# Kernel optimization log

Measured on AMD Instinct MI355X. Metric: run time of the kernel, lower is better.

## Reference

```python
import jax, jax.numpy as jnp
import numpy as np

N = 262144   # total nodes
E = 1048576  # total edges
B = 512      # graphs per batch
IN, H, EDIM, AH, CH, NB = 8, 128, 4, 128, 128, 4

def _lin(key, fi, fo):
    # kaiming_normal fan_out/relu approximated with fan_in scaling (only affects init stats)
    return jax.random.normal(key, (fi, fo), jnp.float32) * np.sqrt(2.0 / fi)

def setup_inputs() -> dict:
    key = jax.random.key(0)
    ks = jax.random.split(key, 24)
    inp = {}
    inp['x'] = jax.random.normal(ks[0], (N, IN), jnp.float32)
    inp['edge_index'] = jax.random.randint(ks[1], (2, E), 0, N)
    inp['edge_attr'] = jax.random.normal(ks[2], (E, EDIM), jnp.float32)
    seg = N // B
    inp['batch'] = (jnp.arange(N) // seg).astype(jnp.int32)
    inp['ptr'] = (jnp.arange(B + 1) * seg).astype(jnp.int32)
    dims = [(IN, H), (H, H), (H, H)]  # final layer outputs embed_dim == H
    for l, (di, do) in enumerate(dims):
        inp[f'We{l}'] = _lin(ks[3 + 2 * l], EDIM, di)
        inp[f'be{l}'] = jnp.zeros((di,), jnp.float32)
        inp[f'W{l}'] = _lin(ks[4 + 2 * l], di, do)
        inp[f'b{l}'] = jnp.zeros((do,), jnp.float32)
    inp['laW1'] = _lin(ks[10], H, AH); inp['lab1'] = jnp.zeros((AH,), jnp.float32)
    inp['laW2'] = _lin(ks[11], AH, 1); inp['lab2'] = jnp.zeros((1,), jnp.float32)
    inp['maW1'] = _lin(ks[12], H, AH); inp['mab1'] = jnp.zeros((AH,), jnp.float32)
    inp['maW2'] = _lin(ks[13], AH, NB); inp['mab2'] = jnp.zeros((NB,), jnp.float32)
    inp['lcW1'] = _lin(ks[14], H, CH); inp['lcb1'] = jnp.zeros((CH,), jnp.float32)
    inp['lcW2'] = _lin(ks[15], CH, 1); inp['lcb2'] = jnp.zeros((1,), jnp.float32)
    inp['mcW1'] = _lin(ks[16], H, CH); inp['mcb1'] = jnp.zeros((CH,), jnp.float32)
    inp['mcW2'] = _lin(ks[17], CH, 1); inp['mcb2'] = jnp.zeros((1,), jnp.float32)
    return inp

def _gnn(x, edge_index, edge_attr, Wes, bes, Ws, bs):
    # GINE-style edge-conditioned message passing (dropout off / eval mode)
    src, dst = edge_index[0], edge_index[1]
    h = x
    for We, be, W, b in zip(Wes, bes, Ws, bs):
        msg = jax.nn.relu(h[src] + edge_attr @ We + be)            # [E, d]
        agg = jax.ops.segment_sum(msg, dst, num_segments=N)        # [N, d]
        h = jax.nn.relu((h + agg) @ W + b)
    return h

def reference(x, edge_index, edge_attr, batch, ptr,
              We0, be0, W0, b0, We1, be1, W1, b1, We2, be2, W2, b2,
              laW1, lab1, laW2, lab2, maW1, mab1, maW2, mab2,
              lcW1, lcb1, lcW2, lcb2, mcW1, mcb1, mcW2, mcb2):
    emb = _gnn(x, edge_index, edge_attr, [We0, We1, We2], [be0, be1, be2], [W0, W1, W2], [b0, b1, b2])  # [N, H]

    # per-node location logit, then fused segmented softmax over each graph's nodes
    loc_logits = (jax.nn.relu(emb @ laW1 + lab1) @ laW2 + lab2)[:, 0]  # [N]
    seg_max = jax.ops.segment_max(loc_logits, batch, num_segments=B)
    shifted = loc_logits - seg_max[batch]
    denom = jax.ops.segment_sum(jnp.exp(shifted), batch, num_segments=B)
    logp = shifted - jnp.log(denom)[batch]                              # per-node log-prob within its graph
    loc_entropy = -jax.ops.segment_sum(jnp.exp(logp) * logp, batch, num_segments=B)  # [B]

    # segmented categorical sampling via Gumbel-max (global node index, matching start+local_idx)
    key = jax.random.key(42)
    u = jax.random.uniform(key, (N,), minval=1e-6, maxval=1.0 - 1e-6)
    pert = loc_logits - jnp.log(-jnp.log(u))
    pmax = jax.ops.segment_max(pert, batch, num_segments=B)
    cand = jnp.where(pert >= pmax[batch], jnp.arange(N), N)
    locations = jax.ops.segment_min(cand, batch, num_segments=B)        # [B] global indices
    loc_log_probs = logp[locations]                                     # [B]

    sel = emb[locations]                                                # [B, H]
    mut_logits = jax.nn.relu(sel @ maW1 + mab1) @ maW2 + mab2           # [B, NB]
    mut_logp = jax.nn.log_softmax(mut_logits, axis=-1)
    mutations = jax.random.categorical(jax.random.fold_in(key, 1), mut_logits, axis=-1)  # [B]
    mut_log_probs = jnp.take_along_axis(mut_logp, mutations[:, None], axis=-1)[:, 0]
    mut_entropy = -jnp.sum(jnp.exp(mut_logp) * mut_logp, axis=-1)

    # critics: global_add_pool + MLP -> scalar per graph; mutation critic on selected node
    pooled = jax.ops.segment_sum(emb, batch, num_segments=B)            # [B, H]
    loc_values = (jax.nn.relu(pooled @ lcW1 + lcb1) @ lcW2 + lcb2)[:, 0]
    mut_values = (jax.nn.relu(sel @ mcW1 + mcb1) @ mcW2 + mcb2)[:, 0]

    return (locations, mutations, loc_log_probs, mut_log_probs,
            loc_entropy, mut_entropy, loc_values, mut_values, emb)
```

## Files before the change

### kernel.cpp

```cpp
#include <hip/hip_runtime.h>
#include <cstdint>
#include <cstddef>

#define NN 262144
#define EE 1048576
#define BB 512
#define SEG 512

__device__ __forceinline__ unsigned rotl32(unsigned x, int r) {
    return (x << r) | (x >> (32 - r));
}

__device__ __forceinline__ void tf2x32(unsigned k0, unsigned k1, unsigned x0, unsigned x1,
                                       unsigned& o0, unsigned& o1) {
    unsigned ks[3] = {k0, k1, k0 ^ k1 ^ 0x1BD11BDAu};
    x0 += ks[0]; x1 += ks[1];
    const int R0[4] = {13, 15, 26, 6};
    const int R1[4] = {17, 29, 16, 24};
#pragma unroll
    for (int i = 0; i < 5; ++i) {
        const int* R = (i & 1) ? R1 : R0;
#pragma unroll
        for (int j = 0; j < 4; ++j) {
            x0 += x1;
            x1 = rotl32(x1, R[j]);
            x1 ^= x0;
        }
        x0 += ks[(i + 1) % 3];
        x1 += ks[(i + 2) % 3] + (unsigned)(i + 1);
    }
    o0 = x0; o1 = x1;
}

__device__ __forceinline__ float unif_loc(unsigned idx) {
    unsigned j = idx & (NN / 2 - 1);
    unsigned half = idx >> 17;
    unsigned o0, o1;
    tf2x32(0u, 42u, j, j + (unsigned)(NN / 2), o0, o1);
    unsigned bits = half ? o1 : o0;
    float f = __uint_as_float((bits >> 9) | 0x3F800000u) - 1.0f;
    const float minv = 1e-6f;
    const float maxv = 1.0f - 1e-6f;
    const float span = maxv - minv;
    return fmaxf(minv, __fadd_rn(__fmul_rn(f, span), minv));
}

__global__ void csr_count(const int* __restrict__ dst, int* __restrict__ counts, int E) {
    int i = blockIdx.x * 256 + threadIdx.x;
    if (i < E) atomicAdd(&counts[dst[i]], 1);
}

__global__ void scan512(const int* __restrict__ in, int* __restrict__ outExcl, int* __restrict__ bsum) {
    __shared__ int s[512];
    int b = blockIdx.x, tid = threadIdx.x;
    int v = in[(size_t)b * 512 + tid];
    s[tid] = v;
    __syncthreads();
    for (int d = 1; d < 512; d <<= 1) {
        int add = (tid >= d) ? s[tid - d] : 0;
        __syncthreads();
        s[tid] += add;
        __syncthreads();
    }
    outExcl[(size_t)b * 512 + tid] = s[tid] - v;
    if (tid == 511) bsum[b] = s[511];
}

__global__ void scan_fix(int* __restrict__ offs, const int* __restrict__ bbase,
                         int* __restrict__ cursor, int N, int E) {
    int gid = blockIdx.x * 512 + threadIdx.x;
    int v = offs[gid] + bbase[blockIdx.x];
    offs[gid] = v;
    cursor[gid] = v;
    if (gid == 0) offs[N] = E;
}

__global__ void csr_fill(const int* __restrict__ dst, const int* __restrict__ src,
                         const float4* __restrict__ ea, int* __restrict__ cursor,
                         int* __restrict__ ssrc, float4* __restrict__ sea, int E) {
    int i = blockIdx.x * 256 + threadIdx.x;
    if (i < E) {
        int p = atomicAdd(&cursor[dst[i]], 1);
        ssrc[p] = src[i];
        sea[p] = ea[i];
    }
}

__global__ void agg_l0(const float* __restrict__ x, const int* __restrict__ ssrc,
                       const float4* __restrict__ sea, const int* __restrict__ offs,
                       const float* __restrict__ We0, const float* __restrict__ be0,
                       float* __restrict__ out) {
    __shared__ float Ws[32];
    __shared__ float bs[8];
    int tid = threadIdx.x;
    if (tid < 32) Ws[tid] = We0[tid];
    if (tid < 8) bs[tid] = be0[tid];
    __syncthreads();
    int n = blockIdx.x * 256 + tid;
    float a[8] = {0.f, 0.f, 0.f, 0.f, 0.f, 0.f, 0.f, 0.f};
    int pb = offs[n], pe = offs[n + 1];
    for (int p = pb; p < pe; ++p) {
        int s = ssrc[p];
        float4 ev = sea[p];
        float4 xa = *(const float4*)(x + (size_t)s * 8);
        float4 xb = *(const float4*)(x + (size_t)s * 8 + 4);
        float xs[8] = {xa.x, xa.y, xa.z, xa.w, xb.x, xb.y, xb.z, xb.w};
#pragma unroll
        for (int j2 = 0; j2 < 8; ++j2) {
            float m = xs[j2] + bs[j2] + ev.x * Ws[j2] + ev.y * Ws[8 + j2] +
                      ev.z * Ws[16 + j2] + ev.w * Ws[24 + j2];
            a[j2] += fmaxf(m, 0.f);
        }
    }
    float4 o0 = {a[0], a[1], a[2], a[3]};
    float4 o1 = {a[4], a[5], a[6], a[7]};
    *(float4*)(out + (size_t)n * 8) = o0;
    *(float4*)(out + (size_t)n * 8 + 4) = o1;
}

__global__ void update_l0(const float* __restrict__ x, const float* __restrict__ agg0,
                          const float* __restrict__ W0, const float* __restrict__ b0,
                          float* __restrict__ h1) {
    __shared__ float Ws[8 * 128];
    __shared__ float bs[128];
    __shared__ float ts[2][8];
    int tid = threadIdx.x;
#pragma unroll
    for (int i = tid; i < 1024; i += 256) Ws[i] = W0[i];
    if (tid < 128) bs[tid] = b0[tid];
    int sub = tid >> 7;
    int c = tid & 127;
    int node = blockIdx.x * 2 + sub;
    if (c < 8) ts[sub][c] = x[(size_t)node * 8 + c] + agg0[(size_t)node * 8 + c];
    __syncthreads();
    float acc = bs[c];
#pragma unroll
    for (int k = 0; k < 8; ++k) acc = fmaf(ts[sub][k], Ws[k * 128 + c], acc);
    h1[(size_t)node * 128 + c] = fmaxf(acc, 0.f);
}

#define MSG(hv, ev)                                                                 \
    {                                                                               \
        float mx = hv.x + bv.x + ev.x * w0.x + ev.y * w1.x + ev.z * w2.x + ev.w * w3.x; \
        float my = hv.y + bv.y + ev.x * w0.y + ev.y * w1.y + ev.z * w2.y + ev.w * w3.y; \
        acc.x += fmaxf(mx, 0.f);                                                    \
        acc.y += fmaxf(my, 0.f);                                                    \
    }

__global__ __launch_bounds__(256) void agg_l(const float2* __restrict__ h2,
                                             const int* __restrict__ ssrc,
                                             const float4* __restrict__ sea,
                                             const int* __restrict__ offs,
                                             const float* __restrict__ We,
                                             const float* __restrict__ be,
                                             float2* __restrict__ out) {
    int tid = threadIdx.x;
    int node = blockIdx.x * 4 + (tid >> 6);
    node = __builtin_amdgcn_readfirstlane(node);
    int lane = tid & 63;
    const float2* We2 = (const float2*)We;
    float2 w0 = We2[lane], w1 = We2[64 + lane], w2 = We2[128 + lane], w3 = We2[192 + lane];
    float2 bv = ((const float2*)be)[lane];
    float2 acc; acc.x = 0.f; acc.y = 0.f;
    int pb = offs[node], pe = offs[node + 1];
    int p = pb;
    for (; p + 4 <= pe; p += 4) {
        int s0 = ssrc[p], s1 = ssrc[p + 1], s2 = ssrc[p + 2], s3 = ssrc[p + 3];
        float4 e0 = sea[p], e1 = sea[p + 1], e2 = sea[p + 2], e3 = sea[p + 3];
        float2 ha = h2[(size_t)s0 * 64 + lane];
        float2 hb = h2[(size_t)s1 * 64 + lane];
        float2 hc = h2[(size_t)s2 * 64 + lane];
        float2 hd = h2[(size_t)s3 * 64 + lane];
        MSG(ha, e0) MSG(hb, e1) MSG(hc, e2) MSG(hd, e3)
    }
    for (; p < pe; ++p) {
        int s0 = ssrc[p];
        float4 e0 = sea[p];
        float2 ha = h2[(size_t)s0 * 64 + lane];
        MSG(ha, e0)
    }
    out[(size_t)node * 64 + lane] = acc;
}

__device__ __forceinline__ int wslot(int c) {
    return (c & 1) ? (16 + (((c >> 1) + 4) & 15)) : (c >> 1);
}

__global__ __launch_bounds__(256, 4) void gemm_k(const float* __restrict__ P, const float* Q,
                                                 const float* __restrict__ W,
                                                 const float* __restrict__ bias,
                                                 float* out) {
    __shared__ float As[32][132];
    __shared__ float Ws[32][128];
    int tid = threadIdx.x;
    int r0 = blockIdx.x * 128;
    int ty = tid >> 4, tx = tid & 15;
    int wo1 = 4 * tx;
    int wo2 = 64 + 4 * ((tx + 4) & 15);
    float acc[8][8] = {};
    for (int kc = 0; kc < 4; ++kc) {
        int k0 = kc * 32;
        __syncthreads();
#pragma unroll
        for (int i = 0; i < 4; ++i) {
            int f = tid + 256 * i;
            int r = f >> 3;
            int c4 = f & 7;
            size_t g = (size_t)(r0 + r) * 128 + k0 + 4 * c4;
            float4 pv = *(const float4*)(P + g);
            if (Q) {
                float4 qv = *(const float4*)(Q + g);
                pv.x += qv.x; pv.y += qv.y; pv.z += qv.z; pv.w += qv.w;
            }
            As[4 * c4 + 0][r] = pv.x;
            As[4 * c4 + 1][r] = pv.y;
            As[4 * c4 + 2][r] = pv.z;
            As[4 * c4 + 3][r] = pv.w;
        }
#pragma unroll
        for (int i = 0; i < 4; ++i) {
            int f = tid + 256 * i;
            int k = f >> 5;
            int c4 = f & 31;
            float4 wv = *(const float4*)(W + (size_t)(k0 + k) * 128 + 4 * c4);
            *(float4*)&Ws[k][4 * wslot(c4)] = wv;
        }
        __syncthreads();
#pragma unroll 4
        for (int k = 0; k < 32; ++k) {
            float4 a0 = *(const float4*)&As[k][8 * ty];
            float4 a1 = *(const float4*)&As[k][8 * ty + 4];
            float4 wv0 = *(const float4*)&Ws[k][wo1];
            float4 wv1 = *(const float4*)&Ws[k][wo2];
            float av[8] = {a0.x, a0.y, a0.z, a0.w, a1.x, a1.y, a1.z, a1.w};
            float wv[8] = {wv0.x, wv0.y, wv0.z, wv0.w, wv1.x, wv1.y, wv1.z, wv1.w};
#pragma unroll
            for (int m = 0; m < 8; ++m)
#pragma unroll
                for (int n = 0; n < 8; ++n)
                    acc[m][n] = fmaf(av[m], wv[n], acc[m][n]);
        }
    }
    float4 b0 = *(const float4*)(bias + 8 * tx);
    float4 b1 = *(const float4*)(bias + 8 * tx + 4);
#pragma unroll
    for (int m = 0; m < 8; ++m) {
        float4 o0, o1;
        o0.x = fmaxf(acc[m][0] + b0.x, 0.f);
        o0.y = fmaxf(acc[m][1] + b0.y, 0.f);
        o0.z = fmaxf(acc[m][2] + b0.z, 0.f);
        o0.w = fmaxf(acc[m][3] + b0.w, 0.f);
        o1.x = fmaxf(acc[m][4] + b1.x, 0.f);
        o1.y = fmaxf(acc[m][5] + b1.y, 0.f);
        o1.z = fmaxf(acc[m][6] + b1.z, 0.f);
        o1.w = fmaxf(acc[m][7] + b1.w, 0.f);
        size_t g = (size_t)(r0 + 8 * ty + m) * 128 + 8 * tx;
        *(float4*)(out + g) = o0;
        *(float4*)(out + g + 4) = o1;
    }
}

__global__ __launch_bounds__(256, 4) void gemm_logit(const float* __restrict__ P,
                                                     const float* __restrict__ W,
                                                     const float* __restrict__ bias,
                                                     const float* __restrict__ w2,
                                                     const float* __restrict__ b2,
                                                     float* __restrict__ L) {
    __shared__ float As[32][132];
    __shared__ float Ws[32][128];
    int tid = threadIdx.x;
    int r0 = blockIdx.x * 128;
    int ty = tid >> 4, tx = tid & 15;
    int wo1 = 4 * tx;
    int wo2 = 64 + 4 * ((tx + 4) & 15);
    float acc[8][8] = {};
    for (int kc = 0; kc < 4; ++kc) {
        int k0 = kc * 32;
        __syncthreads();
#pragma unroll
        for (int i = 0; i < 4; ++i) {
            int f = tid + 256 * i;
            int r = f >> 3;
            int c4 = f & 7;
            size_t g = (size_t)(r0 + r) * 128 + k0 + 4 * c4;
            float4 pv = *(const float4*)(P + g);
            As[4 * c4 + 0][r] = pv.x;
            As[4 * c4 + 1][r] = pv.y;
            As[4 * c4 + 2][r] = pv.z;
            As[4 * c4 + 3][r] = pv.w;
        }
#pragma unroll
        for (int i = 0; i < 4; ++i) {
            int f = tid + 256 * i;
            int k = f >> 5;
            int c4 = f & 31;
            float4 wv = *(const float4*)(W + (size_t)(k0 + k) * 128 + 4 * c4);
            *(float4*)&Ws[k][4 * wslot(c4)] = wv;
        }
        __syncthreads();
#pragma unroll 4
        for (int k = 0; k < 32; ++k) {
            float4 a0 = *(const float4*)&As[k][8 * ty];
            float4 a1 = *(const float4*)&As[k][8 * ty + 4];
            float4 wv0 = *(const float4*)&Ws[k][wo1];
            float4 wv1 = *(const float4*)&Ws[k][wo2];
            float av[8] = {a0.x, a0.y, a0.z, a0.w, a1.x, a1.y, a1.z, a1.w};
            float wv[8] = {wv0.x, wv0.y, wv0.z, wv0.w, wv1.x, wv1.y, wv1.z, wv1.w};
#pragma unroll
            for (int m = 0; m < 8; ++m)
#pragma unroll
                for (int n = 0; n < 8; ++n)
                    acc[m][n] = fmaf(av[m], wv[n], acc[m][n]);
        }
    }
    float4 b0 = *(const float4*)(bias + 8 * tx);
    float4 b1 = *(const float4*)(bias + 8 * tx + 4);
    float4 w2a = *(const float4*)(w2 + 8 * tx);
    float4 w2b = *(const float4*)(w2 + 8 * tx + 4);
    float b2v = b2[0];
#pragma unroll
    for (int m = 0; m < 8; ++m) {
        float v = fmaxf(acc[m][0] + b0.x, 0.f) * w2a.x;
        v += fmaxf(acc[m][1] + b0.y, 0.f) * w2a.y;
        v += fmaxf(acc[m][2] + b0.z, 0.f) * w2a.z;
        v += fmaxf(acc[m][3] + b0.w, 0.f) * w2a.w;
        v += fmaxf(acc[m][4] + b1.x, 0.f) * w2b.x;
        v += fmaxf(acc[m][5] + b1.y, 0.f) * w2b.y;
        v += fmaxf(acc[m][6] + b1.z, 0.f) * w2b.z;
        v += fmaxf(acc[m][7] + b1.w, 0.f) * w2b.w;
        v += __shfl_down(v, 8, 16);
        v += __shfl_down(v, 4, 16);
        v += __shfl_down(v, 2, 16);
        v += __shfl_down(v, 1, 16);
        if (tx == 0) L[r0 + 8 * ty + m] = v + b2v;
    }
}

__global__ void sample_k(const float* __restrict__ L, float* __restrict__ ob,
                         int* __restrict__ locInt) {
    int g = blockIdx.x, tid = threadIdx.x;
    __shared__ float sh[512];
    __shared__ float rb[256];
    __shared__ int ib[256];
    float l0 = L[g * 512 + tid];
    float l1 = L[g * 512 + 256 + tid];
    rb[tid] = fmaxf(l0, l1);
    __syncthreads();
    for (int s2 = 128; s2 > 0; s2 >>= 1) {
        if (tid < s2) rb[tid] = fmaxf(rb[tid], rb[tid + s2]);
        __syncthreads();
    }
    float mx = rb[0];
    __syncthreads();
    float s0 = l0 - mx, s1 = l1 - mx;
    sh[tid] = s0; sh[256 + tid] = s1;
    float e0 = expf(s0), e1 = expf(s1);
    rb[tid] = e0 + e1;
    __syncthreads();
    for (int s2 = 128; s2 > 0; s2 >>= 1) {
        if (tid < s2) rb[tid] += rb[tid + s2];
        __syncthreads();
    }
    float denom = rb[0];
    __syncthreads();
    rb[tid] = e0 * s0 + e1 * s1;
    __syncthreads();
    for (int s2 = 128; s2 > 0; s2 >>= 1) {
        if (tid < s2) rb[tid] += rb[tid + s2];
        __syncthreads();
    }
    float sum2 = rb[0];
    __syncthreads();
    unsigned i0 = (unsigned)(g * 512 + tid);
    unsigned i1 = i0 + 256u;
    float p0 = l0 - logf(-logf(unif_loc(i0)));
    float p1 = l1 - logf(-logf(unif_loc(i1)));
    rb[tid] = fmaxf(p0, p1);
    __syncthreads();
    for (int s2 = 128; s2 > 0; s2 >>= 1) {
        if (tid < s2) rb[tid] = fmaxf(rb[tid], rb[tid + s2]);
        __syncthreads();
    }
    float pmax = rb[0];
    __syncthreads();
    int c0 = (p0 >= pmax) ? tid : 0x7FFFFFFF;
    int c1 = (p1 >= pmax) ? (tid + 256) : 0x7FFFFFFF;
    ib[tid] = min(c0, c1);
    __syncthreads();
    for (int s2 = 128; s2 > 0; s2 >>= 1) {
        if (tid < s2) ib[tid] = min(ib[tid], ib[tid + s2]);
        __syncthreads();
    }
    if (tid == 0) {
        int li = ib[0];
        float logD = logf(denom);
        ob[g] = (float)(g * 512 + li);
        ob[1024 + g] = sh[li] - logD;
        ob[2048 + g] = logD - sum2 / denom;
        locInt[g] = g * 512 + li;
    }
}

__global__ void pool_k(const float* __restrict__ emb, float* __restrict__ pooled) {
    int g = blockIdx.x, tid = threadIdx.x;
    int c = tid & 127, rg = tid >> 7;
    __shared__ float sh[512];
    float s0 = 0.f, s1 = 0.f, s2 = 0.f, s3 = 0.f;
    const float* base = emb + ((size_t)g * 512 + (size_t)rg * 128) * 128 + c;
    for (int n = 0; n < 128; n += 4) {
        s0 += base[(size_t)(n + 0) * 128];
        s1 += base[(size_t)(n + 1) * 128];
        s2 += base[(size_t)(n + 2) * 128];
        s3 += base[(size_t)(n + 3) * 128];
    }
    sh[tid] = (s0 + s1) + (s2 + s3);
    __syncthreads();
    if (rg == 0) pooled[g * 128 + c] = sh[c] + sh[128 + c] + sh[256 + c] + sh[384 + c];
}

__global__ void heads_k(const float* __restrict__ emb, const float* __restrict__ pooled,
                        const int* __restrict__ locInt,
                        const float* __restrict__ maW1, const float* __restrict__ mab1,
                        const float* __restrict__ maW2, const float* __restrict__ mab2,
                        const float* __restrict__ lcW1, const float* __restrict__ lcb1,
                        const float* __restrict__ lcW2, const float* __restrict__ lcb2,
                        const float* __restrict__ mcW1, const float* __restrict__ mcb1,
                        const float* __restrict__ mcW2, const float* __restrict__ mcb2,
                        float* __restrict__ ob) {
    int g = blockIdx.x, tid = threadIdx.x;
    __shared__ float sel[128], pl[128];
    __shared__ float red[4][128];
    __shared__ float red1[128];
    __shared__ float mcv_sh;
    sel[tid] = emb[(size_t)locInt[g] * 128 + tid];
    pl[tid] = pooled[g * 128 + tid];
    __syncthreads();
    float h = mab1[tid];
    for (int k = 0; k < 128; ++k) h = fmaf(sel[k], maW1[k * 128 + tid], h);
    h = fmaxf(h, 0.f);
    red[0][tid] = h * maW2[tid * 4 + 0];
    red[1][tid] = h * maW2[tid * 4 + 1];
    red[2][tid] = h * maW2[tid * 4 + 2];
    red[3][tid] = h * maW2[tid * 4 + 3];
    __syncthreads();
    for (int s2 = 64; s2 > 0; s2 >>= 1) {
        if (tid < s2) {
            red[0][tid] += red[0][tid + s2];
            red[1][tid] += red[1][tid + s2];
            red[2][tid] += red[2][tid + s2];
            red[3][tid] += red[3][tid + s2];
        }
        __syncthreads();
    }
    float h2 = mcb1[tid];
    for (int k = 0; k < 128; ++k) h2 = fmaf(sel[k], mcW1[k * 128 + tid], h2);
    h2 = fmaxf(h2, 0.f);
    red1[tid] = h2 * mcW2[tid];
    __syncthreads();
    for (int s2 = 64; s2 > 0; s2 >>= 1) {
        if (tid < s2) red1[tid] += red1[tid + s2];
        __syncthreads();
    }
    if (tid == 0) mcv_sh = red1[0] + mcb2[0];
    __syncthreads();
    float h3 = lcb1[tid];
    for (int k = 0; k < 128; ++k) h3 = fmaf(pl[k], lcW1[k * 128 + tid], h3);
    h3 = fmaxf(h3, 0.f);
    red1[tid] = h3 * lcW2[tid];
    __syncthreads();
    for (int s2 = 64; s2 > 0; s2 >>= 1) {
        if (tid < s2) red1[tid] += red1[tid + s2];
        __syncthreads();
    }
    if (tid == 0) {
        float lcv = red1[0] + lcb2[0];
        float lg[4];
#pragma unroll
        for (int c = 0; c < 4; ++c) lg[c] = red[c][0] + mab2[c];
        unsigned fk0, fk1;
        tf2x32(0u, 42u, 0u, 1u, fk0, fk1);
        float gmb[4];
#pragma unroll
        for (int c = 0; c < 4; ++c) {
            unsigned m = (unsigned)(g * 4 + c);
            unsigned j = m & 1023u;
            unsigned halfb = m >> 10;
            unsigned o0, o1;
            tf2x32(fk0, fk1, j, j + 1024u, o0, o1);
            unsigned bits = halfb ? o1 : o0;
            float f = __uint_as_float((bits >> 9) | 0x3F800000u) - 1.0f;
            const float tiny = 1.17549435e-38f;
            float u = fmaxf(tiny, __fadd_rn(__fmul_rn(f, 1.0f), tiny));
            gmb[c] = -logf(-logf(u));
        }
        int best = 0;
        float bz = gmb[0] + lg[0];
#pragma unroll
        for (int c = 1; c < 4; ++c) {
            float z = gmb[c] + lg[c];
            if (z > bz) { bz = z; best = c; }
        }
        float M = fmaxf(fmaxf(lg[0], lg[1]), fmaxf(lg[2], lg[3]));
        float se = 0.f;
#pragma unroll
        for (int c = 0; c < 4; ++c) se += expf(lg[c] - M);
        float lse = M + logf(se);
        float ent = 0.f;
#pragma unroll
        for (int c = 0; c < 4; ++c) {
            float lp = lg[c] - lse;
            ent -= expf(lp) * lp;
        }
        ob[512 + g] = (float)best;
        ob[1536 + g] = lg[best] - lse;
        ob[2560 + g] = ent;
        ob[3072 + g] = lcv;
        ob[3584 + g] = mcv_sh;
    }
}

extern "C" void kernel_launch(void* const* d_in, const int* in_sizes, int n_in,
                              void* d_out, int out_size, void* d_ws, size_t ws_size,
                              hipStream_t stream) {
    const float* x   = (const float*)d_in[0];
    const int* ei    = (const int*)d_in[1];
    const float* ea  = (const float*)d_in[2];
    const float* We0 = (const float*)d_in[5];
    const float* be0 = (const float*)d_in[6];
    const float* W0  = (const float*)d_in[7];
    const float* b0  = (const float*)d_in[8];
    const float* We1 = (const float*)d_in[9];
    const float* be1 = (const float*)d_in[10];
    const float* W1  = (const float*)d_in[11];
    const float* b1  = (const float*)d_in[12];
    const float* We2 = (const float*)d_in[13];
    const float* be2 = (const float*)d_in[14];
    const float* W2  = (const float*)d_in[15];
    const float* b2  = (const float*)d_in[16];
    const float* laW1 = (const float*)d_in[17];
    const float* lab1 = (const float*)d_in[18];
    const float* laW2 = (const float*)d_in[19];
    const float* lab2 = (const float*)d_in[20];
    const float* maW1 = (const float*)d_in[21];
    const float* mab1 = (const float*)d_in[22];
    const float* maW2 = (const float*)d_in[23];
    const float* mab2 = (const float*)d_in[24];
    const float* lcW1 = (const float*)d_in[25];
    const float* lcb1 = (const float*)d_in[26];
    const float* lcW2 = (const float*)d_in[27];
    const float* lcb2 = (const float*)d_in[28];
    const float* mcW1 = (const float*)d_in[29];
    const float* mcb1 = (const float*)d_in[30];
    const float* mcW2 = (const float*)d_in[31];
    const float* mcb2 = (const float*)d_in[32];

    float* out = (float*)d_out;
    char* ws = (char*)d_ws;
    size_t off = 0;
    auto alloc = [&](size_t bytes) -> void* {
        void* p = ws + off;
        off += (bytes + 255) & ~(size_t)255;
        return p;
    };
    float* U    = (float*)alloc((size_t)NN * 128 * 4);
    int* counts = (int*)alloc((size_t)NN * 4);
    int* offs   = (int*)alloc((size_t)(NN + 1) * 4);
    int* cursor = (int*)alloc((size_t)NN * 4);
    int* ssrc   = (int*)alloc((size_t)EE * 4);
    float4* sea = (float4*)alloc((size_t)EE * 16);
    int* bsum   = (int*)alloc(512 * 4);
    int* bbase  = (int*)alloc(512 * 4);
    int* bscr   = (int*)alloc(512 * 4);
    float* Lg   = (float*)alloc((size_t)NN * 4);
    float* pooled = (float*)alloc((size_t)BB * 128 * 4);
    int* locInt = (int*)alloc((size_t)BB * 4);

    const int* src = ei;
    const int* dstA = ei + EE;
    float* V = out + 4096;
    float* agg0 = U;

    hipMemsetAsync(counts, 0, (size_t)NN * 4, stream);
    csr_count<<<EE / 256, 256, 0, stream>>>(dstA, counts, EE);
    scan512<<<NN / 512, 512, 0, stream>>>(counts, offs, bsum);
    scan512<<<1, 512, 0, stream>>>(bsum, bbase, bscr);
    scan_fix<<<NN / 512, 512, 0, stream>>>(offs, bbase, cursor, NN, EE);
    csr_fill<<<EE / 256, 256, 0, stream>>>(dstA, src, (const float4*)ea, cursor, ssrc, sea, EE);

    agg_l0<<<NN / 256, 256, 0, stream>>>(x, ssrc, sea, offs, We0, be0, agg0);
    update_l0<<<NN / 2, 256, 0, stream>>>(x, agg0, W0, b0, V);
    agg_l<<<NN / 4, 256, 0, stream>>>((const float2*)V, ssrc, sea, offs, We1, be1, (float2*)U);
    gemm_k<<<NN / 128, 256, 0, stream>>>(V, U, W1, b1, U);
    agg_l<<<NN / 4, 256, 0, stream>>>((const float2*)U, ssrc, sea, offs, We2, be2, (float2*)V);
    gemm_k<<<NN / 128, 256, 0, stream>>>(U, V, W2, b2, V);

    gemm_logit<<<NN / 128, 256, 0, stream>>>(V, laW1, lab1, laW2, lab2, Lg);
    sample_k<<<BB, 256, 0, stream>>>(Lg, out, locInt);

    pool_k<<<BB, 512, 0, stream>>>(V, pooled);
    heads_k<<<BB, 128, 0, stream>>>(V, pooled, locInt, maW1, mab1, maW2, mab2,
                                    lcW1, lcb1, lcW2, lcb2, mcW1, mcb1, mcW2, mcb2, out);
}
```

Before: 1.016 ms.

## Replace FP32 FMA GEMMs with split-bf16 MFMA kernels and prepacked weights

The three 128x128 node GEMMs (two layer updates and the location-logit head) now run on MFMA 16x16x32 bf16 instructions instead of scalar FP32 FMA tiles in shared memory. Each operand is split into a high and a low bf16 part and combined with three MFMAs (bf16x3) to stay close to FP32 accuracy. A small pack kernel writes the weights once in fragment order into the now-unused cursor buffer, so the GEMMs read B fragments straight from global/L2 and need no shared memory. A fragments are converted in registers. The cost is extra MFMA work, a small precision loss, and uncoalesced scalar stores in the epilogue.

Measured after the change: 927.3 us. -8.7%, faster.

```diff
diff --git a/kernel.cpp b/kernel.cpp
--- a/kernel.cpp
+++ b/kernel.cpp
@@ -182,158 +182,190 @@
     out[(size_t)node * 64 + lane] = acc;
 }
 
-__device__ __forceinline__ int wslot(int c) {
-    return (c & 1) ? (16 + (((c >> 1) + 4) & 15)) : (c >> 1);
-}
-
-__global__ __launch_bounds__(256, 4) void gemm_k(const float* __restrict__ P, const float* Q,
-                                                 const float* __restrict__ W,
+
+typedef __attribute__((ext_vector_type(8))) short bf16x8;
+typedef __attribute__((ext_vector_type(4))) float f32x4;
+
+__device__ __forceinline__ ushort bf16r(float x) {
+    unsigned u = __float_as_uint(x);
+    return (ushort)((u + 0x7FFFu + ((u >> 16) & 1u)) >> 16);
+}
+__device__ __forceinline__ float bf2f(ushort h) {
+    return __uint_as_float(((unsigned)h) << 16);
+}
+
+__global__ void pack3(const float* __restrict__ W1, const float* __restrict__ W2,
+                      const float* __restrict__ LA, uint4* __restrict__ dst) {
+    const float* W = (blockIdx.x == 0) ? W1 : (blockIdx.x == 1) ? W2 : LA;
+    uint4* ph = dst + (size_t)blockIdx.x * 4096;
+    uint4* pl = ph + 2048;
+    int t = threadIdx.x;
+    int l = t & 63, q = t >> 6;
+    int lo = l & 15, kg = l >> 4;
+    for (int i = 0; i < 8; ++i) {
+        int combo = q * 8 + i;
+        int kc = combo >> 3, n = combo & 7;
+        ushort h8[8], l8[8];
+#pragma unroll
+        for (int j = 0; j < 8; ++j) {
+            float wv = W[(size_t)(kc * 32 + kg * 8 + j) * 128 + n * 16 + lo];
+            ushort hh = bf16r(wv);
+            h8[j] = hh;
+            l8[j] = bf16r(wv - bf2f(hh));
+        }
+        int idx = (kc * 8 + n) * 64 + l;
+        ph[idx] = *(const uint4*)h8;
+        pl[idx] = *(const uint4*)l8;
+    }
+}
+
+__device__ __forceinline__ void load_a_frags(const float* P, const float* Q, int r0,
+                                             int lo, int kg, int kc,
+                                             bf16x8& ah0, bf16x8& al0,
+                                             bf16x8& ah1, bf16x8& al1) {
+#pragma unroll
+    for (int m = 0; m < 2; ++m) {
+        const float* ap = P + (size_t)(r0 + m * 16 + lo) * 128 + kc * 32 + kg * 8;
+        float4 p0 = *(const float4*)ap;
+        float4 p1 = *(const float4*)(ap + 4);
+        if (Q) {
+            const float* qp = Q + (size_t)(r0 + m * 16 + lo) * 128 + kc * 32 + kg * 8;
+            float4 q0 = *(const float4*)qp;
+            float4 q1 = *(const float4*)(qp + 4);
+            p0.x += q0.x; p0.y += q0.y; p0.z += q0.z; p0.w += q0.w;
+            p1.x += q1.x; p1.y += q1.y; p1.z += q1.z; p1.w += q1.w;
+        }
+        float av[8] = {p0.x, p0.y, p0.z, p0.w, p1.x, p1.y, p1.z, p1.w};
+        bf16x8 ah, al;
+#pragma unroll
+        for (int j = 0; j < 8; ++j) {
+            ushort hh = bf16r(av[j]);
+            ah[j] = (short)hh;
+            al[j] = (short)bf16r(av[j] - bf2f(hh));
+        }
+        if (m == 0) { ah0 = ah; al0 = al; } else { ah1 = ah; al1 = al; }
+    }
+}
+
+__global__ __launch_bounds__(256) void gemm_mfma(const float* __restrict__ P, const float* Q,
+                                                 const uint4* __restrict__ Wh,
+                                                 const uint4* __restrict__ Wl,
                                                  const float* __restrict__ bias,
                                                  float* out) {
-    __shared__ float As[32][132];
-    __shared__ float Ws[32][128];
     int tid = threadIdx.x;
-    int r0 = blockIdx.x * 128;
-    int ty = tid >> 4, tx = tid & 15;
-    int wo1 = 4 * tx;
-    int wo2 = 64 + 4 * ((tx + 4) & 15);
-    float acc[8][8] = {};
+    int w = tid >> 6, l = tid & 63;
+    int r0 = blockIdx.x * 128 + w * 32;
+    int lo = l & 15, kg = l >> 4;
+    const bf16x8* Bh = (const bf16x8*)Wh;
+    const bf16x8* Bl = (const bf16x8*)Wl;
+    f32x4 acc[2][8];
+#pragma unroll
+    for (int m = 0; m < 2; ++m)
+#pragma unroll
+        for (int n = 0; n < 8; ++n) acc[m][n] = (f32x4){0.f, 0.f, 0.f, 0.f};
+
     for (int kc = 0; kc < 4; ++kc) {
-        int k0 = kc * 32;
-        __syncthreads();
-#pragma unroll
-        for (int i = 0; i < 4; ++i) {
-            int f = tid + 256 * i;
-            int r = f >> 3;
-            int c4 = f & 7;
-            size_t g = (size_t)(r0 + r) * 128 + k0 + 4 * c4;
-            float4 pv = *(const float4*)(P + g);
-            if (Q) {
-                float4 qv = *(const float4*)(Q + g);
-                pv.x += qv.x; pv.y += qv.y; pv.z += qv.z; pv.w += qv.w;
+        bf16x8 ah0, al0, ah1, al1;
+        load_a_frags(P, Q, r0, lo, kg, kc, ah0, al0, ah1, al1);
+#pragma unroll
+        for (int h2i = 0; h2i < 2; ++h2i) {
+            bf16x8 bh[4], bl[4];
+#pragma unroll
+            for (int nn = 0; nn < 4; ++nn) {
+                int idx = (kc * 8 + h2i * 4 + nn) * 64 + l;
+                bh[nn] = Bh[idx];
+                bl[nn] = Bl[idx];
             }
-            As[4 * c4 + 0][r] = pv.x;
-            As[4 * c4 + 1][r] = pv.y;
-            As[4 * c4 + 2][r] = pv.z;
-            As[4 * c4 + 3][r] = pv.w;
-        }
-#pragma unroll
-        for (int i = 0; i < 4; ++i) {
-            int f = tid + 256 * i;
-            int k = f >> 5;
-            int c4 = f & 31;
-            float4 wv = *(const float4*)(W + (size_t)(k0 + k) * 128 + 4 * c4);
-            *(float4*)&Ws[k][4 * wslot(c4)] = wv;
-        }
-        __syncthreads();
-#pragma unroll 4
-        for (int k = 0; k < 32; ++k) {
-            float4 a0 = *(const float4*)&As[k][8 * ty];
-            float4 a1 = *(const float4*)&As[k][8 * ty + 4];
-            float4 wv0 = *(const float4*)&Ws[k][wo1];
-            float4 wv1 = *(const float4*)&Ws[k][wo2];
-            float av[8] = {a0.x, a0.y, a0.z, a0.w, a1.x, a1.y, a1.z, a1.w};
-            float wv[8] = {wv0.x, wv0.y, wv0.z, wv0.w, wv1.x, wv1.y, wv1.z, wv1.w};
-#pragma unroll
-            for (int m = 0; m < 8; ++m)
-#pragma unroll
-                for (int n = 0; n < 8; ++n)
-                    acc[m][n] = fmaf(av[m], wv[n], acc[m][n]);
-        }
-    }
-    float4 b0 = *(const float4*)(bias + 8 * tx);
-    float4 b1 = *(const float4*)(bias + 8 * tx + 4);
-#pragma unroll
-    for (int m = 0; m < 8; ++m) {
-        float4 o0, o1;
-        o0.x = fmaxf(acc[m][0] + b0.x, 0.f);
-        o0.y = fmaxf(acc[m][1] + b0.y, 0.f);
-        o0.z = fmaxf(acc[m][2] + b0.z, 0.f);
-        o0.w = fmaxf(acc[m][3] + b0.w, 0.f);
-        o1.x = fmaxf(acc[m][4] + b1.x, 0.f);
-        o1.y = fmaxf(acc[m][5] + b1.y, 0.f);
-        o1.z = fmaxf(acc[m][6] + b1.z, 0.f);
-        o1.w = fmaxf(acc[m][7] + b1.w, 0.f);
-        size_t g = (size_t)(r0 + 8 * ty + m) * 128 + 8 * tx;
-        *(float4*)(out + g) = o0;
-        *(float4*)(out + g + 4) = o1;
-    }
-}
-
-__global__ __launch_bounds__(256, 4) void gemm_logit(const float* __restrict__ P,
-                                                     const float* __restrict__ W,
-                                                     const float* __restrict__ bias,
-                                                     const float* __restrict__ w2,
-                                                     const float* __restrict__ b2,
-                                                     float* __restrict__ L) {
-    __shared__ float As[32][132];
-    __shared__ float Ws[32][128];
+#pragma unroll
+            for (int nn = 0; nn < 4; ++nn) {
+                int n = h2i * 4 + nn;
+                acc[0][n] = __builtin_amdgcn_mfma_f32_16x16x32_bf16(ah0, bh[nn], acc[0][n], 0, 0, 0);
+                acc[0][n] = __builtin_amdgcn_mfma_f32_16x16x32_bf16(al0, bh[nn], acc[0][n], 0, 0, 0);
+                acc[0][n] = __builtin_amdgcn_mfma_f32_16x16x32_bf16(ah0, bl[nn], acc[0][n], 0, 0, 0);
+                acc[1][n] = __builtin_amdgcn_mfma_f32_16x16x32_bf16(ah1, bh[nn], acc[1][n], 0, 0, 0);
+                acc[1][n] = __builtin_amdgcn_mfma_f32_16x16x32_bf16(al1, bh[nn], acc[1][n], 0, 0, 0);
+                acc[1][n] = __builtin_amdgcn_mfma_f32_16x16x32_bf16(ah1, bl[nn], acc[1][n], 0, 0, 0);
+            }
+        }
+    }
+    float bv[8];
+#pragma unroll
+    for (int n = 0; n < 8; ++n) bv[n] = bias[n * 16 + lo];
+#pragma unroll
+    for (int m = 0; m < 2; ++m)
+#pragma unroll
+        for (int n = 0; n < 8; ++n)
+#pragma unroll
+            for (int v = 0; v < 4; ++v) {
+                size_t g = (size_t)(r0 + m * 16 + kg * 4 + v) * 128 + n * 16 + lo;
+                out[g] = fmaxf(acc[m][n][v] + bv[n], 0.f);
+            }
+}
+
+__global__ __launch_bounds__(256) void gemm_logit_mfma(const float* __restrict__ P,
+                                                       const uint4* __restrict__ Wh,
+                                                       const uint4* __restrict__ Wl,
+                                                       const float* __restrict__ bias,
+                                                       const float* __restrict__ w2,
+                                                       const float* __restrict__ b2,
+                                                       float* __restrict__ L) {
     int tid = threadIdx.x;
-    int r0 = blockIdx.x * 128;
-    int ty = tid >> 4, tx = tid & 15;
-    int wo1 = 4 * tx;
-    int wo2 = 64 + 4 * ((tx + 4) & 15);
-    float acc[8][8] = {};
+    int w = tid >> 6, l = tid & 63;
+    int r0 = blockIdx.x * 128 + w * 32;
+    int lo = l & 15, kg = l >> 4;
+    const bf16x8* Bh = (const bf16x8*)Wh;
+    const bf16x8* Bl = (const bf16x8*)Wl;
+    f32x4 acc[2][8];
+#pragma unroll
+    for (int m = 0; m < 2; ++m)
+#pragma unroll
+        for (int n = 0; n < 8; ++n) acc[m][n] = (f32x4){0.f, 0.f, 0.f, 0.f};
+
     for (int kc = 0; kc < 4; ++kc) {
-        int k0 = kc * 32;
-        __syncthreads();
-#pragma unroll
-        for (int i = 0; i < 4; ++i) {
-            int f = tid + 256 * i;
-            int r = f >> 3;
-            int c4 = f & 7;
-            size_t g = (size_t)(r0 + r) * 128 + k0 + 4 * c4;
-            float4 pv = *(const float4*)(P + g);
-            As[4 * c4 + 0][r] = pv.x;
-            As[4 * c4 + 1][r] = pv.y;
-            As[4 * c4 + 2][r] = pv.z;
-            As[4 * c4 + 3][r] = pv.w;
-        }
-#pragma unroll
-        for (int i = 0; i < 4; ++i) {
-            int f = tid + 256 * i;
-            int k = f >> 5;
-            int c4 = f & 31;
-            float4 wv = *(const float4*)(W + (size_t)(k0 + k) * 128 + 4 * c4);
-            *(float4*)&Ws[k][4 * wslot(c4)] = wv;
-        }
-        __syncthreads();
-#pragma unroll 4
-        for (int k = 0; k < 32; ++k) {
-            float4 a0 = *(const float4*)&As[k][8 * ty];
-            float4 a1 = *(const float4*)&As[k][8 * ty + 4];
-            float4 wv0 = *(const float4*)&Ws[k][wo1];
-            float4 wv1 = *(const float4*)&Ws[k][wo2];
-            float av[8] = {a0.x, a0.y, a0.z, a0.w, a1.x, a1.y, a1.z, a1.w};
-            float wv[8] = {wv0.x, wv0.y, wv0.z, wv0.w, wv1.x, wv1.y, wv1.z, wv1.w};
-#pragma unroll
-            for (int m = 0; m < 8; ++m)
-#pragma unroll
-                for (int n = 0; n < 8; ++n)
-                    acc[m][n] = fmaf(av[m], wv[n], acc[m][n]);
-        }
-    }
-    float4 b0 = *(const float4*)(bias + 8 * tx);
-    float4 b1 = *(const float4*)(bias + 8 * tx + 4);
-    float4 w2a = *(const float4*)(w2 + 8 * tx);
-    float4 w2b = *(const float4*)(w2 + 8 * tx + 4);
+        bf16x8 ah0, al0, ah1, al1;
+        load_a_frags(P, (const float*)0, r0, lo, kg, kc, ah0, al0, ah1, al1);
+#pragma unroll
+        for (int h2i = 0; h2i < 2; ++h2i) {
+            bf16x8 bh[4], bl[4];
+#pragma unroll
+            for (int nn = 0; nn < 4; ++nn) {
+                int idx = (kc * 8 + h2i * 4 + nn) * 64 + l;
+                bh[nn] = Bh[idx];
+                bl[nn] = Bl[idx];
+            }
+#pragma unroll
+            for (int nn = 0; nn < 4; ++nn) {
+                int n = h2i * 4 + nn;
+                acc[0][n] = __builtin_amdgcn_mfma_f32_16x16x32_bf16(ah0, bh[nn], acc[0][n], 0, 0, 0);
+                acc[0][n] = __builtin_amdgcn_mfma_f32_16x16x32_bf16(al0, bh[nn], acc[0][n], 0, 0, 0);
+                acc[0][n] = __builtin_amdgcn_mfma_f32_16x16x32_bf16(ah0, bl[nn], acc[0][n], 0, 0, 0);
+                acc[1][n] = __builtin_amdgcn_mfma_f32_16x16x32_bf16(ah1, bh[nn], acc[1][n], 0, 0, 0);
+                acc[1][n] = __builtin_amdgcn_mfma_f32_16x16x32_bf16(al1, bh[nn], acc[1][n], 0, 0, 0);
+                acc[1][n] = __builtin_amdgcn_mfma_f32_16x16x32_bf16(ah1, bl[nn], acc[1][n], 0, 0, 0);
+            }
+        }
+    }
+    float bv[8], w2v[8];
+#pragma unroll
+    for (int n = 0; n < 8; ++n) {
+        bv[n] = bias[n * 16 + lo];
+        w2v[n] = w2[n * 16 + lo];
+    }
     float b2v = b2[0];
 #pragma unroll
-    for (int m = 0; m < 8; ++m) {
-        float v = fmaxf(acc[m][0] + b0.x, 0.f) * w2a.x;
-        v += fmaxf(acc[m][1] + b0.y, 0.f) * w2a.y;
-        v += fmaxf(acc[m][2] + b0.z, 0.f) * w2a.z;
-        v += fmaxf(acc[m][3] + b0.w, 0.f) * w2a.w;
-        v += fmaxf(acc[m][4] + b1.x, 0.f) * w2b.x;
-        v += fmaxf(acc[m][5] + b1.y, 0.f) * w2b.y;
-        v += fmaxf(acc[m][6] + b1.z, 0.f) * w2b.z;
-        v += fmaxf(acc[m][7] + b1.w, 0.f) * w2b.w;
-        v += __shfl_down(v, 8, 16);
-        v += __shfl_down(v, 4, 16);
-        v += __shfl_down(v, 2, 16);
-        v += __shfl_down(v, 1, 16);
-        if (tx == 0) L[r0 + 8 * ty + m] = v + b2v;
-    }
+    for (int m = 0; m < 2; ++m)
+#pragma unroll
+        for (int v = 0; v < 4; ++v) {
+            float s = 0.f;
+#pragma unroll
+            for (int n = 0; n < 8; ++n)
+                s += fmaxf(acc[m][n][v] + bv[n], 0.f) * w2v[n];
+            s += __shfl_xor(s, 8);
+            s += __shfl_xor(s, 4);
+            s += __shfl_xor(s, 2);
+            s += __shfl_xor(s, 1);
+            if (lo == 0) L[r0 + m * 16 + kg * 4 + v] = s + b2v;
+        }
 }
 
 __global__ void sample_k(const float* __restrict__ L, float* __restrict__ ob,
@@ -580,21 +612,24 @@
     float* V = out + 4096;
     float* agg0 = U;
 
+    uint4* wpack = (uint4*)cursor;
+
     hipMemsetAsync(counts, 0, (size_t)NN * 4, stream);
     csr_count<<<EE / 256, 256, 0, stream>>>(dstA, counts, EE);
     scan512<<<NN / 512, 512, 0, stream>>>(counts, offs, bsum);
     scan512<<<1, 512, 0, stream>>>(bsum, bbase, bscr);
     scan_fix<<<NN / 512, 512, 0, stream>>>(offs, bbase, cursor, NN, EE);
     csr_fill<<<EE / 256, 256, 0, stream>>>(dstA, src, (const float4*)ea, cursor, ssrc, sea, EE);
+    pack3<<<3, 256, 0, stream>>>(W1, W2, laW1, wpack);
 
     agg_l0<<<NN / 256, 256, 0, stream>>>(x, ssrc, sea, offs, We0, be0, agg0);
     update_l0<<<NN / 2, 256, 0, stream>>>(x, agg0, W0, b0, V);
     agg_l<<<NN / 4, 256, 0, stream>>>((const float2*)V, ssrc, sea, offs, We1, be1, (float2*)U);
-    gemm_k<<<NN / 128, 256, 0, stream>>>(V, U, W1, b1, U);
+    gemm_mfma<<<NN / 128, 256, 0, stream>>>(V, U, wpack, wpack + 2048, b1, U);
     agg_l<<<NN / 4, 256, 0, stream>>>((const float2*)U, ssrc, sea, offs, We2, be2, (float2*)V);
-    gemm_k<<<NN / 128, 256, 0, stream>>>(U, V, W2, b2, V);
-
-    gemm_logit<<<NN / 128, 256, 0, stream>>>(V, laW1, lab1, laW2, lab2, Lg);
+    gemm_mfma<<<NN / 128, 256, 0, stream>>>(U, V, wpack + 4096, wpack + 6144, b2, V);
+
+    gemm_logit_mfma<<<NN / 128, 256, 0, stream>>>(V, wpack + 8192, wpack + 10240, lab1, laW2, lab2, Lg);
     sample_k<<<BB, 256, 0, stream>>>(Lg, out, locInt);
 
     pool_k<<<BB, 512, 0, stream>>>(V, pooled);
```
